# Performance work log

Hardware: AMD Instinct MI355X
Metric: run time of the kernel (lower is better)

Reference implementation:

```python
import jax, jax.numpy as jnp
import numpy as np

N = 50000  # nodes
E = 1600000  # edges
L = 2  # layers
D = 128  # input/hidden dim


def setup_inputs() -> dict:
    key = jax.random.key(0)
    ks = jax.random.split(key, 8)
    s = 1.0 / np.sqrt(D)
    return {
        "x": jax.random.normal(ks[0], (N, D), jnp.float32),
        "edge_index": jax.random.randint(ks[1], (2, E), 0, N, jnp.int64),
        "h": jax.random.normal(ks[2], (L, N, D), jnp.float32),
        "Wx": jax.random.normal(ks[3], (L, 3, D, D), jnp.float32) * s,
        "bx": jax.random.normal(ks[4], (L, 3, D), jnp.float32) * 0.01,
        "Wh": jax.random.normal(ks[5], (L, 3, D, D), jnp.float32) * s,
        "bh": jax.random.normal(ks[6], (L, 3, D), jnp.float32) * 0.01,
    }


def _gcn(x, W, b, src, dst, dinv):
    # GCNConv with added self-loops and symmetric normalization:
    # out = D^{-1/2} (A + I) D^{-1/2} X W + b
    hw = x @ W                                   # [N, H]
    norm = dinv[src] * dinv[dst]                 # [E]
    msg = hw[src] * norm[:, None]                # [E, H]
    agg = jax.ops.segment_sum(msg, dst, num_segments=N)
    agg = agg + hw * (dinv * dinv)[:, None]      # self-loop contribution
    return agg + b


def reference(x, edge_index, h, Wx, bx, Wh, bh):
    src = edge_index[0]
    dst = edge_index[1]
    # in-degree on destination nodes, including self-loop (+1)
    deg = jax.ops.segment_sum(jnp.ones((E,), x.dtype), dst, num_segments=N) + 1.0
    dinv = jax.lax.rsqrt(deg)

    outs = []
    inp = x
    for l in range(L):
        hl = h[l]
        z = jax.nn.sigmoid(_gcn(inp, Wx[l, 0], bx[l, 0], src, dst, dinv)
                           + _gcn(hl, Wh[l, 0], bh[l, 0], src, dst, dinv))
        r = jax.nn.sigmoid(_gcn(inp, Wx[l, 1], bx[l, 1], src, dst, dinv)
                           + _gcn(hl, Wh[l, 1], bh[l, 1], src, dst, dinv))
        h_tilde = jnp.tanh(_gcn(inp, Wx[l, 2], bx[l, 2], src, dst, dinv)
                           + _gcn(r * hl, Wh[l, 2], bh[l, 2], src, dst, dinv))
        out = z * hl + (1.0 - z) * h_tilde
        outs.append(out)
        inp = out
    return jnp.stack(outs, axis=0)  # [L, N, H]
```

## Files before the change

kernel.cpp:

```cpp
#include <hip/hip_runtime.h>

typedef __attribute__((ext_vector_type(8))) unsigned short us8;
typedef __attribute__((ext_vector_type(8))) short s8;
typedef __attribute__((ext_vector_type(4))) float f4;
typedef __attribute__((ext_vector_type(2))) float f2;

#define DEV static __device__ __forceinline__
#define CAP 128
#define NRG 128
#define NBB 256
#define SEGC 128

DEV float bf2f(unsigned short h){ return __uint_as_float(((unsigned)h)<<16); }
DEV unsigned short f2bf(float f){
  unsigned x = __float_as_uint(f);
  x += 0x7fffu + ((x>>16)&1u);
  return (unsigned short)(x>>16);
}
DEV float sigm(float x){ return 1.f/(1.f + __expf(-x)); }

__global__ __launch_bounds__(256) void k_bucket(const int* __restrict__ src,
    const int* __restrict__ dst, unsigned* __restrict__ buf,
    int* __restrict__ cnt2, int e, int n){
  __shared__ int lcnt[NRG];
  int b = blockIdx.x;
  for(int i=threadIdx.x;i<NRG;i+=256) lcnt[i] = 0;
  __syncthreads();
  int chunk = (e + NBB - 1)/NBB;
  int lo = b*chunk;
  int hi = lo + chunk; if(hi>e) hi=e;
  for(int i = lo + threadIdx.x; i < hi; i += 256){
    int d = dst[i], s = src[i];
    int r = (d*NRG)/n;
    int pos = atomicAdd(&lcnt[r], 1);
    if(pos < SEGC)
      buf[((size_t)r*NBB + b)*SEGC + pos] = ((unsigned)d<<16) | (unsigned)s;
  }
  __syncthreads();
  for(int i=threadIdx.x;i<NRG;i+=256) cnt2[i*NBB + b] = lcnt[i];
}

__global__ __launch_bounds__(256) void k_build2(const unsigned* __restrict__ buf,
    const int* __restrict__ cnt2, int* __restrict__ cnt,
    unsigned short* __restrict__ col, int n){
  int r = blockIdx.x;
  int lo = (r*n + NRG-1)/NRG;
  int hi = ((r+1)*n + NRG-1)/NRG;
  int span = hi - lo;
  __shared__ int lc[512];
  for(int i=threadIdx.x; i<span; i+=256) lc[i] = 0;
  __syncthreads();
  int lane = threadIdx.x & 63;
  for(int seg = threadIdx.x>>6; seg < NBB; seg += 4){
    int c = cnt2[r*NBB + seg]; if(c > SEGC) c = SEGC;
    const unsigned* p = buf + ((size_t)r*NBB + seg)*SEGC;
    for(int i = lane; i < c; i += 64){
      unsigned v = p[i];
      int d = (int)(v >> 16), s = (int)(v & 0xffffu);
      int slot = atomicAdd(&lc[d - lo], 1);
      col[(size_t)d*CAP + slot] = (unsigned short)s;
    }
  }
  __syncthreads();
  for(int i=threadIdx.x; i<span; i+=256) cnt[lo + i] = lc[i];
}

__global__ void k_setup(const int* __restrict__ cnt, float* __restrict__ dinv, int n,
                        const float* __restrict__ Wx, const float* __restrict__ Wh,
                        unsigned short* __restrict__ WT){
  int gN = (n + 255)/256;
  int b = blockIdx.x;
  if(b < gN){
    int i = b*256 + threadIdx.x;
    if(i<n) dinv[i] = rsqrtf((float)cnt[i] + 1.0f);
  } else {
    int i = (b-gN)*256 + threadIdx.x;
    int m = i >> 15;
    int rem = i & 32767;
    int j = rem >> 8;
    int k = rem & 255;
    float v = (k<128) ? Wx[((size_t)m*128 + k)*128 + j]
                      : Wh[((size_t)m*128 + (k-128))*128 + j];
    WT[(size_t)m*32768 + j*256 + k] = f2bf(v);
  }
}

__global__ void k_scale2(const float* __restrict__ inp, const float* __restrict__ hl,
                         const float* __restrict__ dinv, unsigned char* __restrict__ y2, int n){
  int i = blockIdx.x*blockDim.x+threadIdx.x;
  if(i >= n*32) return;
  int node = i>>5, d0 = (i&31)*4;
  float dv = dinv[node];
  f4 a = *(const f4*)(inp + (size_t)node*128 + d0);
  f4 b = *(const f4*)(hl  + (size_t)node*128 + d0);
  unsigned pa = __builtin_amdgcn_cvt_pk_fp8_f32(dv*a[0], dv*a[1], 0, false);
  pa = __builtin_amdgcn_cvt_pk_fp8_f32(dv*a[2], dv*a[3], pa, true);
  unsigned pb = __builtin_amdgcn_cvt_pk_fp8_f32(dv*b[0], dv*b[1], 0, false);
  pb = __builtin_amdgcn_cvt_pk_fp8_f32(dv*b[2], dv*b[3], pb, true);
  *(unsigned*)(y2 + (size_t)node*256 + d0)       = pa;
  *(unsigned*)(y2 + (size_t)node*256 + 128 + d0) = pb;
}

template<int DB>
__global__ __launch_bounds__(256) void k_agg(const unsigned char* __restrict__ y,
    const int* __restrict__ cnt, const unsigned short* __restrict__ col,
    const float* __restrict__ dinv, unsigned short* __restrict__ out0, int n)
{
  constexpr int GL = DB/16;
  constexpr int NG = 64/GL;
  constexpr int U = 8;
  int tid = threadIdx.x;
  int wave = tid>>6, lane = tid&63;
  int g = lane/GL, gl = lane%GL;
  int node = blockIdx.x*(4*NG) + wave*NG + g;
  if(node >= n) return;
  const unsigned char* yb = y + (size_t)gl*16;
  float acc[16];
  {
    uint4 q = *(const uint4*)(yb + (size_t)node*DB);
    const unsigned* qw = (const unsigned*)&q;
    #pragma unroll
    for(int w=0;w<4;++w){
      f2 lo = __builtin_amdgcn_cvt_pk_f32_fp8(qw[w], false);
      f2 hi = __builtin_amdgcn_cvt_pk_f32_fp8(qw[w], true);
      acc[w*4+0]=lo[0]; acc[w*4+1]=lo[1]; acc[w*4+2]=hi[0]; acc[w*4+3]=hi[1];
    }
  }
  const unsigned short* myrow = col + (size_t)node*CAP;
  int c_ = cnt[node];
  int last = c_ - 1;
  for(int i=0; i<c_; i += U){
    int s[U];
    #pragma unroll
    for(int u=0;u<U;++u){
      int ii = i + u; ii = (ii < last) ? ii : last;
      s[u] = myrow[ii];
    }
    uint4 v[U];
    #pragma unroll
    for(int u=0;u<U;++u) v[u] = *(const uint4*)(yb + (size_t)s[u]*DB);
    #pragma unroll
    for(int u=0;u<U;++u){
      if(i + u < c_){
        const unsigned* qw = (const unsigned*)&v[u];
        #pragma unroll
        for(int w=0;w<4;++w){
          f2 lo = __builtin_amdgcn_cvt_pk_f32_fp8(qw[w], false);
          f2 hi = __builtin_amdgcn_cvt_pk_f32_fp8(qw[w], true);
          acc[w*4+0]+=lo[0]; acc[w*4+1]+=lo[1]; acc[w*4+2]+=hi[0]; acc[w*4+3]+=hi[1];
        }
      }
    }
  }
  float dv = dinv[node];
  us8 w0, w1;
  #pragma unroll
  for(int j=0;j<8;++j){ w0[j]=f2bf(acc[j]*dv); w1[j]=f2bf(acc[8+j]*dv); }
  int c = gl*16;
  *(us8*)(out0 + (size_t)node*DB + c)     = w0;
  *(us8*)(out0 + (size_t)node*DB + c + 8) = w1;
}

DEV void stageB256(unsigned char* Bs, const unsigned short* Bsrc, int srcOff, int t){
  #pragma unroll
  for(int i=0;i<8;++i){
    int c = t + i*256;
    int j = c >> 4, kc = c & 15;
    us8 v = *(const us8*)(Bsrc + (size_t)j*256 + srcOff + kc*8);
    *(us8*)(Bs + ((j*256 + kc*16) ^ ((j&7)<<4))) = v;
  }
}
DEV void loadA4(const unsigned short* A, int astride, int arow, int nrows, int hi,
                int koff, s8 (&a)[4]){
  const unsigned short* Ap = A + (size_t)(arow < nrows ? arow : 0)*astride + koff + hi*8;
  #pragma unroll
  for(int kk=0;kk<4;++kk) a[kk] = *(const s8*)(Ap + kk*32);
  if(arow >= nrows){
    #pragma unroll
    for(int kk=0;kk<4;++kk) a[kk] = (s8)(short)0;
  }
}
DEV void mfma128(const unsigned char* Bs, const s8 (&a)[4], int lo, int hi,
                 f4 (&acc)[8]){
  #pragma unroll
  for(int kk=0;kk<4;++kk){
    #pragma unroll
    for(int n=0;n<8;++n){
      int j = n*16+lo;
      s8 b = *(const s8*)(Bs + ((j*256 + kk*64 + hi*16) ^ ((lo&7)<<4)));
      acc[n] = __builtin_amdgcn_mfma_f32_16x16x32_bf16(a[kk], b, acc[n], 0,0,0);
    }
  }
}

__global__ __launch_bounds__(256) void k_gemmRH(
    const unsigned short* __restrict__ axah, const unsigned short* __restrict__ Wr,
    const unsigned short* __restrict__ Wh2, const float* __restrict__ hl,
    const float* __restrict__ dinv, const float* __restrict__ bxr,
    const float* __restrict__ bhr, unsigned char* __restrict__ yq,
    unsigned short* __restrict__ Zbh, int nrows)
{
  __shared__ unsigned char Bs[32768];
  const int t = threadIdx.x, lane = t & 63, lo = lane & 15, hi = lane >> 4;
  const int r0 = blockIdx.x*64 + (t>>6)*16;
  const int arow = r0 + lo;
  s8 a03[4], a47[4];
  f4 accR[8], accH[8];
  #pragma unroll
  for(int n=0;n<8;++n){ accR[n]=(f4)0.f; accH[n]=(f4)0.f; }
  loadA4(axah, 256, arow, nrows, hi, 0, a03);
  stageB256(Bs, Wr, 0, t);
  __syncthreads();
  mfma128(Bs, a03, lo, hi, accR);
  __syncthreads();
  loadA4(axah, 256, arow, nrows, hi, 128, a47);
  stageB256(Bs, Wr, 128, t);
  __syncthreads();
  mfma128(Bs, a47, lo, hi, accR);
  __syncthreads();
  stageB256(Bs, Wh2, 0, t);
  #pragma unroll
  for(int n=0;n<8;++n){
    const int colv = n*16 + lo;
    float bz = bxr[colv] + bhr[colv];
    #pragma unroll
    for(int tt=0;tt<4;++tt){
      int row = r0 + hi*4 + tt;
      if(row < nrows){
        float r = sigm(accR[n][tt] + bz);
        float q = dinv[row] * r * hl[(size_t)row*128 + colv];
        unsigned pk = __builtin_amdgcn_cvt_pk_fp8_f32(q, q, 0, false);
        yq[(size_t)row*128 + colv] = (unsigned char)(pk & 0xff);
      }
    }
  }
  __syncthreads();
  mfma128(Bs, a03, lo, hi, accH);
  #pragma unroll
  for(int n=0;n<8;++n){
    const int colv = n*16 + lo;
    #pragma unroll
    for(int tt=0;tt<4;++tt){
      int row = r0 + hi*4 + tt;
      if(row < nrows) Zbh[(size_t)row*128 + colv] = f2bf(accH[n][tt]);
    }
  }
}

__global__ __launch_bounds__(256) void k_gemmZF(
    const unsigned short* __restrict__ axah, const unsigned short* __restrict__ aq,
    const unsigned short* __restrict__ Wz, const unsigned short* __restrict__ Wh2,
    const unsigned short* __restrict__ Zbh, const float* __restrict__ hl,
    const float* __restrict__ hnext, const float* __restrict__ dinv,
    const float* __restrict__ bxz, const float* __restrict__ bhz,
    const float* __restrict__ bxh, const float* __restrict__ bhh,
    float* __restrict__ outp, unsigned char* __restrict__ y2out, int nrows)
{
  __shared__ unsigned char Bs[32768];
  const int t = threadIdx.x, lane = t & 63, lo = lane & 15, hi = lane >> 4;
  const int r0 = blockIdx.x*64 + (t>>6)*16;
  const int arow = r0 + lo;
  s8 a[4];
  f4 accZ[8], accH[8];
  #pragma unroll
  for(int n=0;n<8;++n){ accZ[n]=(f4)0.f; accH[n]=(f4)0.f; }
  loadA4(axah, 256, arow, nrows, hi, 0, a);
  stageB256(Bs, Wz, 0, t);
  __syncthreads();
  mfma128(Bs, a, lo, hi, accZ);
  __syncthreads();
  loadA4(axah, 256, arow, nrows, hi, 128, a);
  stageB256(Bs, Wz, 128, t);
  __syncthreads();
  mfma128(Bs, a, lo, hi, accZ);
  __syncthreads();
  loadA4(aq, 128, arow, nrows, hi, 0, a);
  stageB256(Bs, Wh2, 128, t);
  __syncthreads();
  mfma128(Bs, a, lo, hi, accH);
  #pragma unroll
  for(int n=0;n<8;++n){
    const int colv = n*16 + lo;
    float bz = bxz[colv] + bhz[colv];
    float bh = bxh[colv] + bhh[colv];
    #pragma unroll
    for(int tt=0;tt<4;++tt){
      int row = r0 + hi*4 + tt;
      if(row >= nrows) continue;
      float z  = sigm(accZ[n][tt] + bz);
      float ht = tanhf(accH[n][tt] + bf2f(Zbh[(size_t)row*128 + colv]) + bh);
      float ov = z*hl[(size_t)row*128 + colv] + (1.f - z)*ht;
      outp[(size_t)row*128 + colv] = ov;
      if(y2out){
        float dv = dinv[row];
        unsigned pk = __builtin_amdgcn_cvt_pk_fp8_f32(dv*ov, dv*ov, 0, false);
        y2out[(size_t)row*256 + colv] = (unsigned char)(pk & 0xff);
        float hv = dv * hnext[(size_t)row*128 + colv];
        unsigned ph = __builtin_amdgcn_cvt_pk_fp8_f32(hv, hv, 0, false);
        y2out[(size_t)row*256 + 128 + colv] = (unsigned char)(ph & 0xff);
      }
    }
  }
}

extern "C" void kernel_launch(void* const* d_in, const int* in_sizes, int n_in,
                              void* d_out, int out_size, void* d_ws, size_t ws_size,
                              hipStream_t stream){
  const float* x  = (const float*)d_in[0];
  const int*   ei = (const int*)d_in[1];
  const float* h  = (const float*)d_in[2];
  const float* Wx = (const float*)d_in[3];
  const float* bx = (const float*)d_in[4];
  const float* Wh = (const float*)d_in[5];
  const float* bh = (const float*)d_in[6];
  float* out = (float*)d_out;

  const int N = in_sizes[0] / 128;
  const int E = in_sizes[1] / 2;
  const int L = in_sizes[2] / in_sizes[0];
  const int* src = ei;
  const int* dst = ei + E;

  char* w = (char*)d_ws;
  auto alloc = [&](size_t b)->char*{ char* p = w; w += (b + 255) & ~(size_t)255; return p; };
  int* cnt = (int*)alloc((size_t)N*sizeof(int));
  unsigned short* col = (unsigned short*)alloc((size_t)N*CAP*sizeof(short));
  float* dinv = (float*)alloc((size_t)N*sizeof(float));
  unsigned short* WT = (unsigned short*)alloc((size_t)6*32768*sizeof(short));
  unsigned char* y2 = (unsigned char*)alloc((size_t)N*256);
  unsigned short* axah = (unsigned short*)alloc((size_t)N*256*sizeof(short));
  unsigned char* yq = (unsigned char*)alloc((size_t)N*128);
  unsigned short* aq = (unsigned short*)alloc((size_t)N*128*sizeof(short));
  unsigned short* Zbh = (unsigned short*)alloc((size_t)N*128*sizeof(short));
  unsigned* ebuf = (unsigned*)alloc((size_t)NRG*NBB*SEGC*sizeof(unsigned));
  int* cnt2 = (int*)alloc((size_t)NRG*NBB*sizeof(int));

  const int gN = (N + 255)/256;
  const int gew = (N*32 + 255)/256;
  const int g64 = (N + 63)/64;
  const int gagg4 = (N + 15)/16;
  const int gagg2 = (N + 31)/32;

  k_bucket<<<NBB,256,0,stream>>>(src, dst, ebuf, cnt2, E, N);
  k_build2<<<NRG,256,0,stream>>>(ebuf, cnt2, cnt, col, N);
  k_setup<<<gN + 768,256,0,stream>>>(cnt, dinv, N, Wx, Wh, WT);

  for(int l=0; l<L; ++l){
    const float* hl  = h + (size_t)l*N*128;
    const float* bxz = bx + (size_t)(l*3+0)*128; const float* bhz = bh + (size_t)(l*3+0)*128;
    const float* bxr = bx + (size_t)(l*3+1)*128; const float* bhr = bh + (size_t)(l*3+1)*128;
    const float* bxh = bx + (size_t)(l*3+2)*128; const float* bhh = bh + (size_t)(l*3+2)*128;
    const unsigned short* Wz = WT + (size_t)(l*3+0)*32768;
    const unsigned short* Wr = WT + (size_t)(l*3+1)*32768;
    const unsigned short* Wh2= WT + (size_t)(l*3+2)*32768;

    if(l==0) k_scale2<<<gew,256,0,stream>>>(x, hl, dinv, y2, N);
    k_agg<256><<<gagg4,256,0,stream>>>(y2, cnt, col, dinv, axah, N);
    k_gemmRH<<<g64,256,0,stream>>>(axah, Wr, Wh2, hl, dinv, bxr, bhr, yq, Zbh, N);
    k_agg<128><<<gagg2,256,0,stream>>>(yq, cnt, col, dinv, aq, N);
    k_gemmZF<<<g64,256,0,stream>>>(axah, aq, Wz, Wh2, Zbh, hl,
        (l+1<L) ? (h + (size_t)(l+1)*N*128) : nullptr, dinv,
        bxz, bhz, bxh, bhh, out + (size_t)l*N*128,
        (l+1<L) ? y2 : nullptr, N);
  }
}
```

Measured before the change: 428.3 us.

## Stage full weights once per block and split GEMM columns across 16 waves

The two gate GEMM kernels now use 1024-thread blocks covering 128 rows. Each block stages the full 256x128 input weight and the 128x128 hidden weight into 96 KB of shared memory up front, then issues a single barrier instead of the repeated stage/sync cycles. Each wave computes half of the output columns, which halves the accumulator registers per wave and amortises weight staging over twice as many rows. The cost is much larger LDS use per block, which limits how many blocks can be resident on each CU, and the bigger blocks reduce scheduling flexibility.

```diff
diff --git a/kernel.cpp b/kernel.cpp
--- a/kernel.cpp
+++ b/kernel.cpp
@@ -161,13 +161,22 @@
   *(us8*)(out0 + (size_t)node*DB + c + 8) = w1;
 }
 
-DEV void stageB256(unsigned char* Bs, const unsigned short* Bsrc, int srcOff, int t){
-  #pragma unroll
-  for(int i=0;i<8;++i){
-    int c = t + i*256;
+DEV void stageB1(unsigned char* Bs1, const unsigned short* W, int t){
+  #pragma unroll
+  for(int i=0;i<4;++i){
+    int c = t + i*1024;
+    int j = c >> 5, kc = c & 31;
+    us8 v = *(const us8*)(W + (size_t)j*256 + kc*8);
+    *(us8*)(Bs1 + ((j*512 + kc*16) ^ ((j&7)<<4))) = v;
+  }
+}
+DEV void stageB2(unsigned char* Bs2, const unsigned short* W, int srcOff, int t){
+  #pragma unroll
+  for(int i=0;i<2;++i){
+    int c = t + i*1024;
     int j = c >> 4, kc = c & 15;
-    us8 v = *(const us8*)(Bsrc + (size_t)j*256 + srcOff + kc*8);
-    *(us8*)(Bs + ((j*256 + kc*16) ^ ((j&7)<<4))) = v;
+    us8 v = *(const us8*)(W + (size_t)j*256 + srcOff + kc*8);
+    *(us8*)(Bs2 + ((j*256 + kc*16) ^ ((j&7)<<4))) = v;
   }
 }
 DEV void loadA4(const unsigned short* A, int astride, int arow, int nrows, int hi,
@@ -180,48 +189,49 @@
     for(int kk=0;kk<4;++kk) a[kk] = (s8)(short)0;
   }
 }
-DEV void mfma128(const unsigned char* Bs, const s8 (&a)[4], int lo, int hi,
-                 f4 (&acc)[8]){
+template<int KROW>
+DEV void mfma4(const unsigned char* Bs, const s8 (&a)[4], int kk0, int jbase,
+               int lo, int hi, f4 (&acc)[4]){
   #pragma unroll
   for(int kk=0;kk<4;++kk){
     #pragma unroll
-    for(int n=0;n<8;++n){
-      int j = n*16+lo;
-      s8 b = *(const s8*)(Bs + ((j*256 + kk*64 + hi*16) ^ ((lo&7)<<4)));
+    for(int n=0;n<4;++n){
+      int j = jbase + n*16 + lo;
+      s8 b = *(const s8*)(Bs + ((j*KROW + (kk0+kk)*64 + hi*16) ^ ((lo&7)<<4)));
       acc[n] = __builtin_amdgcn_mfma_f32_16x16x32_bf16(a[kk], b, acc[n], 0,0,0);
     }
   }
 }
 
-__global__ __launch_bounds__(256) void k_gemmRH(
+__global__ __launch_bounds__(1024) void k_gemmRH(
     const unsigned short* __restrict__ axah, const unsigned short* __restrict__ Wr,
     const unsigned short* __restrict__ Wh2, const float* __restrict__ hl,
     const float* __restrict__ dinv, const float* __restrict__ bxr,
     const float* __restrict__ bhr, unsigned char* __restrict__ yq,
     unsigned short* __restrict__ Zbh, int nrows)
 {
-  __shared__ unsigned char Bs[32768];
+  __shared__ unsigned char Bs1[65536];
+  __shared__ unsigned char Bs2[32768];
   const int t = threadIdx.x, lane = t & 63, lo = lane & 15, hi = lane >> 4;
-  const int r0 = blockIdx.x*64 + (t>>6)*16;
+  const int wid = t >> 6, wrow = wid >> 1, whalf = wid & 1;
+  const int jbase = whalf*64;
+  const int r0 = blockIdx.x*128 + wrow*16;
   const int arow = r0 + lo;
+  stageB1(Bs1, Wr, t);
+  stageB2(Bs2, Wh2, 0, t);
   s8 a03[4], a47[4];
-  f4 accR[8], accH[8];
-  #pragma unroll
-  for(int n=0;n<8;++n){ accR[n]=(f4)0.f; accH[n]=(f4)0.f; }
   loadA4(axah, 256, arow, nrows, hi, 0, a03);
-  stageB256(Bs, Wr, 0, t);
-  __syncthreads();
-  mfma128(Bs, a03, lo, hi, accR);
-  __syncthreads();
   loadA4(axah, 256, arow, nrows, hi, 128, a47);
-  stageB256(Bs, Wr, 128, t);
-  __syncthreads();
-  mfma128(Bs, a47, lo, hi, accR);
-  __syncthreads();
-  stageB256(Bs, Wh2, 0, t);
-  #pragma unroll
-  for(int n=0;n<8;++n){
-    const int colv = n*16 + lo;
+  f4 accR[4], accH[4];
+  #pragma unroll
+  for(int n=0;n<4;++n){ accR[n]=(f4)0.f; accH[n]=(f4)0.f; }
+  __syncthreads();
+  mfma4<512>(Bs1, a03, 0, jbase, lo, hi, accR);
+  mfma4<512>(Bs1, a47, 4, jbase, lo, hi, accR);
+  mfma4<256>(Bs2, a03, 0, jbase, lo, hi, accH);
+  #pragma unroll
+  for(int n=0;n<4;++n){
+    const int colv = jbase + n*16 + lo;
     float bz = bxr[colv] + bhr[colv];
     #pragma unroll
     for(int tt=0;tt<4;++tt){
@@ -231,23 +241,13 @@
         float q = dinv[row] * r * hl[(size_t)row*128 + colv];
         unsigned pk = __builtin_amdgcn_cvt_pk_fp8_f32(q, q, 0, false);
         yq[(size_t)row*128 + colv] = (unsigned char)(pk & 0xff);
+        Zbh[(size_t)row*128 + colv] = f2bf(accH[n][tt]);
       }
     }
   }
-  __syncthreads();
-  mfma128(Bs, a03, lo, hi, accH);
-  #pragma unroll
-  for(int n=0;n<8;++n){
-    const int colv = n*16 + lo;
-    #pragma unroll
-    for(int tt=0;tt<4;++tt){
-      int row = r0 + hi*4 + tt;
-      if(row < nrows) Zbh[(size_t)row*128 + colv] = f2bf(accH[n][tt]);
-    }
-  }
-}
-
-__global__ __launch_bounds__(256) void k_gemmZF(
+}
+
+__global__ __launch_bounds__(1024) void k_gemmZF(
     const unsigned short* __restrict__ axah, const unsigned short* __restrict__ aq,
     const unsigned short* __restrict__ Wz, const unsigned short* __restrict__ Wh2,
     const unsigned short* __restrict__ Zbh, const float* __restrict__ hl,
@@ -256,31 +256,29 @@
     const float* __restrict__ bxh, const float* __restrict__ bhh,
     float* __restrict__ outp, unsigned char* __restrict__ y2out, int nrows)
 {
-  __shared__ unsigned char Bs[32768];
+  __shared__ unsigned char Bs1[65536];
+  __shared__ unsigned char Bs2[32768];
   const int t = threadIdx.x, lane = t & 63, lo = lane & 15, hi = lane >> 4;
-  const int r0 = blockIdx.x*64 + (t>>6)*16;
+  const int wid = t >> 6, wrow = wid >> 1, whalf = wid & 1;
+  const int jbase = whalf*64;
+  const int r0 = blockIdx.x*128 + wrow*16;
   const int arow = r0 + lo;
-  s8 a[4];
-  f4 accZ[8], accH[8];
-  #pragma unroll
-  for(int n=0;n<8;++n){ accZ[n]=(f4)0.f; accH[n]=(f4)0.f; }
-  loadA4(axah, 256, arow, nrows, hi, 0, a);
-  stageB256(Bs, Wz, 0, t);
-  __syncthreads();
-  mfma128(Bs, a, lo, hi, accZ);
-  __syncthreads();
-  loadA4(axah, 256, arow, nrows, hi, 128, a);
-  stageB256(Bs, Wz, 128, t);
-  __syncthreads();
-  mfma128(Bs, a, lo, hi, accZ);
-  __syncthreads();
-  loadA4(aq, 128, arow, nrows, hi, 0, a);
-  stageB256(Bs, Wh2, 128, t);
-  __syncthreads();
-  mfma128(Bs, a, lo, hi, accH);
-  #pragma unroll
-  for(int n=0;n<8;++n){
-    const int colv = n*16 + lo;
+  stageB1(Bs1, Wz, t);
+  stageB2(Bs2, Wh2, 128, t);
+  s8 a03[4], a47[4], aq4[4];
+  loadA4(axah, 256, arow, nrows, hi, 0, a03);
+  loadA4(axah, 256, arow, nrows, hi, 128, a47);
+  loadA4(aq, 128, arow, nrows, hi, 0, aq4);
+  f4 accZ[4], accH[4];
+  #pragma unroll
+  for(int n=0;n<4;++n){ accZ[n]=(f4)0.f; accH[n]=(f4)0.f; }
+  __syncthreads();
+  mfma4<512>(Bs1, a03, 0, jbase, lo, hi, accZ);
+  mfma4<512>(Bs1, a47, 4, jbase, lo, hi, accZ);
+  mfma4<256>(Bs2, aq4, 0, jbase, lo, hi, accH);
+  #pragma unroll
+  for(int n=0;n<4;++n){
+    const int colv = jbase + n*16 + lo;
     float bz = bxz[colv] + bhz[colv];
     float bh = bxh[colv] + bhh[colv];
     #pragma unroll
@@ -337,7 +335,7 @@
 
   const int gN = (N + 255)/256;
   const int gew = (N*32 + 255)/256;
-  const int g64 = (N + 63)/64;
+  const int g128 = (N + 127)/128;
   const int gagg4 = (N + 15)/16;
   const int gagg2 = (N + 31)/32;
 
@@ -356,9 +354,9 @@
 
     if(l==0) k_scale2<<<gew,256,0,stream>>>(x, hl, dinv, y2, N);
     k_agg<256><<<gagg4,256,0,stream>>>(y2, cnt, col, dinv, axah, N);
-    k_gemmRH<<<g64,256,0,stream>>>(axah, Wr, Wh2, hl, dinv, bxr, bhr, yq, Zbh, N);
+    k_gemmRH<<<g128,1024,0,stream>>>(axah, Wr, Wh2, hl, dinv, bxr, bhr, yq, Zbh, N);
     k_agg<128><<<gagg2,256,0,stream>>>(yq, cnt, col, dinv, aq, N);
-    k_gemmZF<<<g64,256,0,stream>>>(axah, aq, Wz, Wh2, Zbh, hl,
+    k_gemmZF<<<g128,1024,0,stream>>>(axah, aq, Wz, Wh2, Zbh, hl,
         (l+1<L) ? (h + (size_t)(l+1)*N*128) : nullptr, dinv,
         bxz, bhz, bxh, bhh, out + (size_t)l*N*128,
         (l+1<L) ? y2 : nullptr, N);
```

After: 400.5 us. -6.5%, faster.
